# Optimization experiments

Hardware: AMD Instinct MI355X
Metric: run time of the kernel (lower is better)

Reference implementation:

```python
import jax, jax.numpy as jnp
import numpy as np

IN_F = 1024
OUT_F = 1024
GRID_SIZE = 8
GRID_LO, GRID_HI = -2.0, 2.0


def _grid_and_inv_denom():
    grid = jnp.linspace(GRID_LO, GRID_HI, GRID_SIZE)  # [G]
    inv_denom = 1.0 / (float((GRID_HI - GRID_LO) / (GRID_SIZE - 1)) + 1e-06)
    return grid, inv_denom


def setup_inputs() -> dict:
    key = jax.random.key(0)
    kx, kw, ks = jax.random.split(key, 3)
    x = jax.random.normal(kx, (4, 2048, IN_F), dtype=jnp.float32)
    # kaiming_uniform_(a=sqrt(5)) on [out,in]: bound = sqrt(6/((1+a^2)*fan_in)) = sqrt(1/fan_in)
    bound = float(np.sqrt(1.0 / IN_F))
    base_w = jax.random.uniform(kw, (OUT_F, IN_F), minval=-bound, maxval=bound, dtype=jnp.float32)
    base_b = jnp.zeros((OUT_F,), dtype=jnp.float32)
    spline_w = 0.02 * jax.random.normal(ks, (OUT_F, IN_F, GRID_SIZE), dtype=jnp.float32)
    return {"x": x, "base_w": base_w, "base_b": base_b, "spline_w": spline_w}


def reference(x, base_w, base_b, spline_w):
    grid, inv_denom = _grid_and_inv_denom()
    lead = x.shape[:-1]
    x_flat = x.reshape(-1, IN_F)  # [B, in]
    # base path: Linear(SiLU(x))
    base_out = jax.nn.silu(x_flat) @ base_w.T + base_b  # [B, out]
    # RBF basis expansion: [B, in, G]
    basis = jnp.exp(-(((x_flat[..., None] - grid) * inv_denom) ** 2))
    spline_out = jnp.einsum('big,oig->bo', basis, spline_w)  # [B, out]
    out = base_out + spline_out
    return out.reshape(*lead, OUT_F)
```

## Files before the change

### kernel.cpp

```cpp
#include <hip/hip_runtime.h>
#include <stdint.h>

namespace {

constexpr int IN_F = 1024;
constexpr int OUT_F = 1024;
constexpr int GSZ = 8;
constexpr int KTOT = IN_F + IN_F * GSZ;
constexpr int BK = 64;
constexpr int NT = KTOT / BK;
constexpr int NBASE = IN_F / BK;

constexpr int BM = 128, BN = 256;
constexpr int NBLK = OUT_F / BN;
constexpr size_t IMG_BYTES = (size_t)BN * BK * 2;
constexpr size_t WS_NEEDED = (size_t)NBLK * NT * IMG_BYTES;

constexpr double H_D     = 4.0 / 7.0;
constexpr double INVD_D  = 1.0 / (H_D + 1e-6);
constexpr double L2E_D   = 1.4426950408889634;
constexpr double SQL2E_D = 1.2011224087864498;
constexpr double CS_D    = INVD_D * SQL2E_D;
constexpr double DLT_D   = H_D * CS_D;

using short8 = __attribute__((ext_vector_type(8))) short;
using f32x4  = __attribute__((ext_vector_type(4))) float;

__device__ __forceinline__ unsigned cvt_pk(float lo, float hi) {
  unsigned r;
  asm("v_cvt_pk_bf16_f32 %0, %1, %2" : "=v"(r) : "v"(lo), "v"(hi));
  return r;
}
__device__ __forceinline__ float silu_f(float v) {
  float e = __builtin_amdgcn_exp2f(-v * (float)L2E_D);
  return v * __builtin_amdgcn_rcpf(1.0f + e);
}
__device__ __forceinline__ int swz(int row, int kk) {
  return (row * 128 + kk * 2) ^ ((row & 7) << 4);
}

__global__ void wprep(const float* __restrict__ bw, const float* __restrict__ sw,
                      char* __restrict__ wimg)
{
  const int total = NBLK * NT * BN * 8;
  for (int idx = blockIdx.x * blockDim.x + threadIdx.x; idx < total;
       idx += gridDim.x * blockDim.x) {
    const int kk8  = idx & 7;
    const int row  = (idx >> 3) & (BN - 1);
    const int rest = idx >> 11;
    const int step = rest % NT;
    const int nb   = rest / NT;
    const int o    = nb * BN + row;
    const int k    = step * BK + kk8 * 8;
    const float* src = (k < IN_F)
      ? (bw + (size_t)o * IN_F + k)
      : (sw + (size_t)o * (size_t)(IN_F * GSZ) + (k - IN_F));
    const float4 a = ((const float4*)src)[0];
    const float4 b = ((const float4*)src)[1];
    int4 v;
    v.x = (int)cvt_pk(a.x, a.y);
    v.y = (int)cvt_pk(a.z, a.w);
    v.z = (int)cvt_pk(b.x, b.y);
    v.w = (int)cvt_pk(b.z, b.w);
    *(int4*)(wimg + (size_t)rest * IMG_BYTES + swz(row, kk8 * 8)) = v;
  }
}

__global__ __launch_bounds__(512, 2)
void kan_fast(const float* __restrict__ x, const float* __restrict__ bb,
              const char* __restrict__ wimg, float* __restrict__ out)
{
  __shared__ char tA[2][BM * BK * 2];
  __shared__ char tB[2][BN * BK * 2];

  const int t    = threadIdx.x;
  const int lane = t & 63;
  const int wid  = t >> 6;
  const int wr   = (wid >> 2) * 64;
  const int wc   = (wid & 3) * 64;
  const int bm0  = blockIdx.y * BM;
  const char* img = wimg + (size_t)blockIdx.x * NT * IMG_BYTES;
  const int bn0  = blockIdx.x * BN;

  const float CSf  = (float)CS_D;
  const float C0f  = (float)(-2.0 * CS_D);
  const float TDLT = (float)(2.0 * DLT_D);
  float Kc[7];
#pragma unroll
  for (int g = 0; g < 7; ++g) {
    const double cg  = (-2.0 + g * H_D) * CS_D;
    const double cg1 = (-2.0 + (g + 1) * H_D) * CS_D;
    Kc[g] = __builtin_amdgcn_exp2f((float)(-DLT_D * (cg + cg1)));
  }

  f32x4 acc[4][4];
#pragma unroll
  for (int m = 0; m < 4; ++m)
#pragma unroll
    for (int n = 0; n < 4; ++n) acc[m][n] = (f32x4)0.0f;

  float4 xE[4], xO[4];

  auto issue_B2 = [&](int step, char* dstB, int half) {
    const char* g = img + (size_t)step * IMG_BYTES + half * 16384 + t * 16;
    char* l = dstB + half * 16384 + t * 16;
#pragma unroll
    for (int j = 0; j < 2; ++j)
      __builtin_amdgcn_global_load_lds(
        (const __attribute__((address_space(1))) void*)(g + j * 8192),
        (__attribute__((address_space(3))) void*)(l + j * 8192), 16, 0, 0);
  };

  auto load_x = [&](int step, float4 (&xr)[4]) {
    const int k0  = step * BK;
    const int row = t >> 2;
    if (k0 < IN_F) {
      const float* p = x + (size_t)(bm0 + row) * IN_F + k0 + (t & 3) * 16;
#pragma unroll
      for (int j = 0; j < 4; ++j) xr[j] = ((const float4*)p)[j];
    } else {
      const int i0 = (k0 - IN_F) >> 3;
      const float2 v = *(const float2*)(x + (size_t)(bm0 + row) * IN_F + i0 + (t & 3) * 2);
      xr[0].x = v.x; xr[0].y = v.y;
    }
  };

  auto conv_A = [&](int step, const float4 (&xr)[4], char* dstA) {
    const int row = t >> 2;
    if (step < NBASE) {
      unsigned q[8];
#pragma unroll
      for (int j = 0; j < 4; ++j) {
        q[2 * j]     = cvt_pk(silu_f(xr[j].x), silu_f(xr[j].y));
        q[2 * j + 1] = cvt_pk(silu_f(xr[j].z), silu_f(xr[j].w));
      }
      const int kc0 = (t & 3) * 16;
      *(int4*)(dstA + swz(row, kc0))     = make_int4(q[0], q[1], q[2], q[3]);
      *(int4*)(dstA + swz(row, kc0 + 8)) = make_int4(q[4], q[5], q[6], q[7]);
    } else {
#pragma unroll
      for (int c = 0; c < 2; ++c) {
        const float xv = c ? xr[0].y : xr[0].x;
        const float tb = xv * CSf;
        const float d0 = tb - C0f;
        float e = __builtin_amdgcn_exp2f(-(d0 * d0));
        const float r = __builtin_amdgcn_exp2f(tb * TDLT);
        unsigned q[4];
#pragma unroll
        for (int g = 0; g < 4; ++g) {
          const float a = e;
          const float b = a * r * Kc[2 * g];
          q[g] = cvt_pk(a, b);
          if (g < 3) e = b * r * Kc[2 * g + 1];
        }
        const int iloc = (t & 3) * 2 + c;
        *(int4*)(dstA + swz(row, iloc * 8)) = make_int4(q[0], q[1], q[2], q[3]);
      }
    }
  };

  auto read_frags = [&](const char* A, const char* B, int kh,
                        short8 (&af)[4], short8 (&bf)[4]) {
    const int r  = lane & 15;
    const int kq = (lane >> 4) * 8;
#pragma unroll
    for (int m = 0; m < 4; ++m)
      af[m] = *(const short8*)(A + swz(wr + m * 16 + r, kh * 32 + kq));
#pragma unroll
    for (int n = 0; n < 4; ++n)
      bf[n] = *(const short8*)(B + swz(wc + n * 16 + r, kh * 32 + kq));
  };

  auto mfma16 = [&](short8 (&af)[4], short8 (&bf)[4]) {
#pragma unroll
    for (int m = 0; m < 4; ++m)
#pragma unroll
      for (int n = 0; n < 4; ++n)
        acc[m][n] = __builtin_amdgcn_mfma_f32_16x16x32_bf16(af[m], bf[n], acc[m][n], 0, 0, 0);
  };

  auto step_body = [&](int s, char* curA, char* curB, char* nxtA, char* nxtB,
                       const float4 (&xconv)[4], float4 (&xload)[4]) {
    if (s + 1 < NT) issue_B2(s + 1, nxtB, 0);
    if (s + 2 < NT) load_x(s + 2, xload);
    {
      short8 af[4], bf[4];
      read_frags(curA, curB, 0, af, bf);
      __builtin_amdgcn_s_barrier();
      asm volatile("s_waitcnt lgkmcnt(0)" ::: "memory");
      __builtin_amdgcn_sched_barrier(0);
      __builtin_amdgcn_s_setprio(1);
      mfma16(af, bf);
      __builtin_amdgcn_s_setprio(0);
      __builtin_amdgcn_s_barrier();
    }
    if (s + 1 < NT) {
      issue_B2(s + 1, nxtB, 1);
      conv_A(s + 1, xconv, nxtA);
    }
    {
      short8 af[4], bf[4];
      read_frags(curA, curB, 1, af, bf);
      __builtin_amdgcn_s_barrier();
      asm volatile("s_waitcnt lgkmcnt(0)" ::: "memory");
      __builtin_amdgcn_sched_barrier(0);
      __builtin_amdgcn_s_setprio(1);
      mfma16(af, bf);
      __builtin_amdgcn_s_setprio(0);
    }
    __syncthreads();
  };

  load_x(0, xE);
  load_x(1, xO);
  issue_B2(0, tB[0], 0);
  issue_B2(0, tB[0], 1);
  conv_A(0, xE, tA[0]);
  __syncthreads();

  for (int s = 0; s < NT; s += 2) {
    step_body(s,     tA[0], tB[0], tA[1], tB[1], xO, xE);
    step_body(s + 1, tA[1], tB[1], tA[0], tB[0], xE, xO);
  }

  const int col = lane & 15;
  const int rr  = (lane >> 4) * 4;
#pragma unroll
  for (int m = 0; m < 4; ++m) {
    const int gr = bm0 + wr + m * 16 + rr;
#pragma unroll
    for (int n = 0; n < 4; ++n) {
      const int gc = bn0 + wc + n * 16 + col;
      const float bias = bb[gc];
#pragma unroll
      for (int j = 0; j < 4; ++j)
        out[(size_t)(gr + j) * OUT_F + gc] = acc[m][n][j] + bias;
    }
  }
}

constexpr int SLDK = 64 + 8;

__device__ __forceinline__ unsigned f2bf(float f) {
  unsigned u = __float_as_uint(f);
  return (u + 0x7fffu + ((u >> 16) & 1u)) >> 16;
}
__device__ __forceinline__ unsigned pk2(float lo, float hi) {
  return f2bf(lo) | (f2bf(hi) << 16);
}

__global__ __launch_bounds__(256)
void kan_slow(const float* __restrict__ x, const float* __restrict__ bw,
              const float* __restrict__ bb, const float* __restrict__ sw,
              float* __restrict__ out)
{
  __shared__ unsigned short tA[128][SLDK];
  __shared__ unsigned short tB[128][SLDK];

  const int t    = threadIdx.x;
  const int lane = t & 63;
  const int wid  = t >> 6;
  const int wr   = (wid >> 1) * 64;
  const int wc   = (wid & 1) * 64;
  const int bm0  = blockIdx.x * 128;
  const int bn0  = blockIdx.y * 128;

  const float CS = (float)CS_D;
  float gsc[GSZ];
#pragma unroll
  for (int g = 0; g < GSZ; ++g)
    gsc[g] = (float)((-2.0 + g * H_D) * CS_D);

  f32x4 acc[4][4];
#pragma unroll
  for (int m = 0; m < 4; ++m)
#pragma unroll
    for (int n = 0; n < 4; ++n) acc[m][n] = (f32x4)0.0f;

  float4 rA[8], rB[8];
  const int rw = t >> 4;
  const int cw = (t & 15) * 4;

  auto load_tile = [&](int step) {
    const int k0 = step * BK;
    const bool base = (k0 < IN_F);
#pragma unroll
    for (int j = 0; j < 8; ++j) {
      const int row = j * 16 + rw;
      const float* p = base
        ? (bw + (size_t)(bn0 + row) * IN_F + k0 + cw)
        : (sw + (size_t)(bn0 + row) * (size_t)(IN_F * GSZ) + (k0 - IN_F) + cw);
      rB[j] = *(const float4*)p;
    }
    if (base) {
#pragma unroll
      for (int j = 0; j < 8; ++j) {
        const int row = j * 16 + rw;
        rA[j] = *(const float4*)(x + (size_t)(bm0 + row) * IN_F + k0 + cw);
      }
    } else {
      const int i0  = (k0 - IN_F) >> 3;
      const int row = t >> 1;
      rA[0] = *(const float4*)(x + (size_t)(bm0 + row) * IN_F + i0 + (t & 1) * 4);
    }
  };

  auto store_tile = [&](int step) {
    const int k0 = step * BK;
    const bool base = (k0 < IN_F);
#pragma unroll
    for (int j = 0; j < 8; ++j) {
      const int row = j * 16 + rw;
      uint2 v;
      v.x = pk2(rB[j].x, rB[j].y);
      v.y = pk2(rB[j].z, rB[j].w);
      *(uint2*)&tB[row][cw] = v;
    }
    if (base) {
#pragma unroll
      for (int j = 0; j < 8; ++j) {
        const int row = j * 16 + rw;
        uint2 v;
        v.x = pk2(silu_f(rA[j].x), silu_f(rA[j].y));
        v.y = pk2(silu_f(rA[j].z), silu_f(rA[j].w));
        *(uint2*)&tA[row][cw] = v;
      }
    } else {
      const int row  = t >> 1;
      const int half = t & 1;
      const float* xv = (const float*)&rA[0];
#pragma unroll
      for (int c = 0; c < 4; ++c) {
        const float tb = xv[c] * CS;
        union { unsigned u[4]; int4 v4; } pkv;
#pragma unroll
        for (int g = 0; g < 8; g += 2) {
          const float t0 = tb - gsc[g];
          const float t1 = tb - gsc[g + 1];
          const float e0 = __builtin_amdgcn_exp2f(-(t0 * t0));
          const float e1 = __builtin_amdgcn_exp2f(-(t1 * t1));
          pkv.u[g >> 1] = pk2(e0, e1);
        }
        const int kc = (half * 4 + c) * 8;
        *(int4*)&tA[row][kc] = pkv.v4;
      }
    }
  };

  auto compute_tile = [&]() {
    const int r  = lane & 15;
    const int kq = (lane >> 4) * 8;
#pragma unroll
    for (int kh = 0; kh < 2; ++kh) {
      short8 af[4], bf[4];
#pragma unroll
      for (int m = 0; m < 4; ++m)
        af[m] = *(const short8*)&tA[wr + m * 16 + r][kh * 32 + kq];
#pragma unroll
      for (int n = 0; n < 4; ++n)
        bf[n] = *(const short8*)&tB[wc + n * 16 + r][kh * 32 + kq];
#pragma unroll
      for (int m = 0; m < 4; ++m)
#pragma unroll
        for (int n = 0; n < 4; ++n)
          acc[m][n] = __builtin_amdgcn_mfma_f32_16x16x32_bf16(af[m], bf[n], acc[m][n], 0, 0, 0);
    }
  };

  load_tile(0);
  for (int step = 0; step < NT; ++step) {
    store_tile(step);
    __syncthreads();
    if (step + 1 < NT) load_tile(step + 1);
    compute_tile();
    __syncthreads();
  }

  const int col = lane & 15;
  const int rr  = (lane >> 4) * 4;
#pragma unroll
  for (int m = 0; m < 4; ++m) {
    const int gr = bm0 + wr + m * 16 + rr;
#pragma unroll
    for (int n = 0; n < 4; ++n) {
      const int gc = bn0 + wc + n * 16 + col;
      const float bias = bb[gc];
#pragma unroll
      for (int j = 0; j < 4; ++j)
        out[(size_t)(gr + j) * OUT_F + gc] = acc[m][n][j] + bias;
    }
  }
}

}

extern "C" void kernel_launch(void* const* d_in, const int* in_sizes, int n_in,
                              void* d_out, int out_size, void* d_ws, size_t ws_size,
                              hipStream_t stream) {
  const float *x, *bw, *bb, *sw;
  if (in_sizes[0] == OUT_F) {
    bb = (const float*)d_in[0];
    bw = (const float*)d_in[1];
    sw = (const float*)d_in[2];
    x  = (const float*)d_in[3];
  } else {
    x  = (const float*)d_in[0];
    bw = (const float*)d_in[1];
    bb = (const float*)d_in[2];
    sw = (const float*)d_in[3];
  }
  float* out = (float*)d_out;
  const int rows = (in_sizes[0] == OUT_F) ? in_sizes[3] / IN_F : in_sizes[0] / IN_F;

  if (ws_size >= WS_NEEDED && d_ws != nullptr && (rows % BM) == 0) {
    hipLaunchKernelGGL(wprep, dim3(2048), dim3(256), 0, stream, bw, sw, (char*)d_ws);
    dim3 grid(NBLK, rows / BM);
    hipLaunchKernelGGL(kan_fast, grid, dim3(512), 0, stream,
                       x, bb, (const char*)d_ws, out);
  } else {
    dim3 grid(rows / 128, OUT_F / 128);
    hipLaunchKernelGGL(kan_slow, grid, dim3(256), 0, stream, x, bw, bb, sw, out);
  }
}
```

Measured before the change: 187.7 us.

## Halve M tile to 64 rows with 4-wave blocks and single-buffered A tile

Shrinks the block tile from 128x256 to 64x256, with 256 threads per block where each wave owns a 64-column slice. This doubles the number of blocks in the grid. The A tile drops from two LDS buffers to one, so the basis/SiLU conversion now runs after the MFMAs behind an extra __syncthreads rather than overlapping with them. B images are loaded in one call per step. The intent is a smaller LDS and register footprint and more blocks for occupancy, at the cost of twice the global B traffic per output and a serialized A-conversion phase.

Result: slower. 203.4 us (+8.4%).

```diff
diff --git a/kernel.cpp b/kernel.cpp
--- a/kernel.cpp
+++ b/kernel.cpp
@@ -11,7 +11,7 @@
 constexpr int NT = KTOT / BK;
 constexpr int NBASE = IN_F / BK;
 
-constexpr int BM = 128, BN = 256;
+constexpr int BM = 64, BN = 256;
 constexpr int NBLK = OUT_F / BN;
 constexpr size_t IMG_BYTES = (size_t)BN * BK * 2;
 constexpr size_t WS_NEEDED = (size_t)NBLK * NT * IMG_BYTES;
@@ -66,18 +66,17 @@
   }
 }
 
-__global__ __launch_bounds__(512, 2)
+__global__ __launch_bounds__(256, 2)
 void kan_fast(const float* __restrict__ x, const float* __restrict__ bb,
               const char* __restrict__ wimg, float* __restrict__ out)
 {
-  __shared__ char tA[2][BM * BK * 2];
+  __shared__ char tA[BM * BK * 2];
   __shared__ char tB[2][BN * BK * 2];
 
   const int t    = threadIdx.x;
   const int lane = t & 63;
   const int wid  = t >> 6;
-  const int wr   = (wid >> 2) * 64;
-  const int wc   = (wid & 3) * 64;
+  const int wc   = wid * 64;
   const int bm0  = blockIdx.y * BM;
   const char* img = wimg + (size_t)blockIdx.x * NT * IMG_BYTES;
   const int bn0  = blockIdx.x * BN;
@@ -101,14 +100,14 @@
 
   float4 xE[4], xO[4];
 
-  auto issue_B2 = [&](int step, char* dstB, int half) {
-    const char* g = img + (size_t)step * IMG_BYTES + half * 16384 + t * 16;
-    char* l = dstB + half * 16384 + t * 16;
-#pragma unroll
-    for (int j = 0; j < 2; ++j)
+  auto issue_B = [&](int step, char* dstB) {
+    const char* g = img + (size_t)step * IMG_BYTES + t * 16;
+    char* l = dstB + t * 16;
+#pragma unroll
+    for (int j = 0; j < 8; ++j)
       __builtin_amdgcn_global_load_lds(
-        (const __attribute__((address_space(1))) void*)(g + j * 8192),
-        (__attribute__((address_space(3))) void*)(l + j * 8192), 16, 0, 0);
+        (const __attribute__((address_space(1))) void*)(g + j * 4096),
+        (__attribute__((address_space(3))) void*)(l + j * 4096), 16, 0, 0);
   };
 
   auto load_x = [&](int step, float4 (&xr)[4]) {
@@ -125,7 +124,7 @@
     }
   };
 
-  auto conv_A = [&](int step, const float4 (&xr)[4], char* dstA) {
+  auto conv_A = [&](int step, const float4 (&xr)[4]) {
     const int row = t >> 2;
     if (step < NBASE) {
       unsigned q[8];
@@ -135,37 +134,44 @@
         q[2 * j + 1] = cvt_pk(silu_f(xr[j].z), silu_f(xr[j].w));
       }
       const int kc0 = (t & 3) * 16;
-      *(int4*)(dstA + swz(row, kc0))     = make_int4(q[0], q[1], q[2], q[3]);
-      *(int4*)(dstA + swz(row, kc0 + 8)) = make_int4(q[4], q[5], q[6], q[7]);
+      *(int4*)(tA + swz(row, kc0))     = make_int4(q[0], q[1], q[2], q[3]);
+      *(int4*)(tA + swz(row, kc0 + 8)) = make_int4(q[4], q[5], q[6], q[7]);
     } else {
-#pragma unroll
-      for (int c = 0; c < 2; ++c) {
-        const float xv = c ? xr[0].y : xr[0].x;
-        const float tb = xv * CSf;
-        const float d0 = tb - C0f;
-        float e = __builtin_amdgcn_exp2f(-(d0 * d0));
-        const float r = __builtin_amdgcn_exp2f(tb * TDLT);
-        unsigned q[4];
-#pragma unroll
-        for (int g = 0; g < 4; ++g) {
-          const float a = e;
-          const float b = a * r * Kc[2 * g];
-          q[g] = cvt_pk(a, b);
-          if (g < 3) e = b * r * Kc[2 * g + 1];
+      float2 xv; xv.x = xr[0].x; xv.y = xr[0].y;
+      float2 tb; tb.x = xv.x * CSf;        tb.y = xv.y * CSf;
+      float2 d0; d0.x = tb.x - C0f;        d0.y = tb.y - C0f;
+      float2 e;
+      e.x = __builtin_amdgcn_exp2f(-(d0.x * d0.x));
+      e.y = __builtin_amdgcn_exp2f(-(d0.y * d0.y));
+      float2 r;
+      r.x = __builtin_amdgcn_exp2f(tb.x * TDLT);
+      r.y = __builtin_amdgcn_exp2f(tb.y * TDLT);
+      unsigned q0[4], q1[4];
+#pragma unroll
+      for (int g = 0; g < 4; ++g) {
+        float2 a = e;
+        float2 b;
+        b.x = a.x * r.x * Kc[2 * g];
+        b.y = a.y * r.y * Kc[2 * g];
+        q0[g] = cvt_pk(a.x, b.x);
+        q1[g] = cvt_pk(a.y, b.y);
+        if (g < 3) {
+          e.x = b.x * r.x * Kc[2 * g + 1];
+          e.y = b.y * r.y * Kc[2 * g + 1];
         }
-        const int iloc = (t & 3) * 2 + c;
-        *(int4*)(dstA + swz(row, iloc * 8)) = make_int4(q[0], q[1], q[2], q[3]);
       }
-    }
-  };
-
-  auto read_frags = [&](const char* A, const char* B, int kh,
-                        short8 (&af)[4], short8 (&bf)[4]) {
+      const int iloc = (t & 3) * 2;
+      *(int4*)(tA + swz(row, iloc * 8))       = make_int4(q0[0], q0[1], q0[2], q0[3]);
+      *(int4*)(tA + swz(row, (iloc + 1) * 8)) = make_int4(q1[0], q1[1], q1[2], q1[3]);
+    }
+  };
+
+  auto read_frags = [&](const char* B, int kh, short8 (&af)[4], short8 (&bf)[4]) {
     const int r  = lane & 15;
     const int kq = (lane >> 4) * 8;
 #pragma unroll
     for (int m = 0; m < 4; ++m)
-      af[m] = *(const short8*)(A + swz(wr + m * 16 + r, kh * 32 + kq));
+      af[m] = *(const short8*)(tA + swz(m * 16 + r, kh * 32 + kq));
 #pragma unroll
     for (int n = 0; n < 4; ++n)
       bf[n] = *(const short8*)(B + swz(wc + n * 16 + r, kh * 32 + kq));
@@ -179,13 +185,13 @@
         acc[m][n] = __builtin_amdgcn_mfma_f32_16x16x32_bf16(af[m], bf[n], acc[m][n], 0, 0, 0);
   };
 
-  auto step_body = [&](int s, char* curA, char* curB, char* nxtA, char* nxtB,
+  auto step_body = [&](int s, char* curB, char* nxtB,
                        const float4 (&xconv)[4], float4 (&xload)[4]) {
-    if (s + 1 < NT) issue_B2(s + 1, nxtB, 0);
+    if (s + 1 < NT) issue_B(s + 1, nxtB);
     if (s + 2 < NT) load_x(s + 2, xload);
     {
       short8 af[4], bf[4];
-      read_frags(curA, curB, 0, af, bf);
+      read_frags(curB, 0, af, bf);
       __builtin_amdgcn_s_barrier();
       asm volatile("s_waitcnt lgkmcnt(0)" ::: "memory");
       __builtin_amdgcn_sched_barrier(0);
@@ -194,13 +200,9 @@
       __builtin_amdgcn_s_setprio(0);
       __builtin_amdgcn_s_barrier();
     }
-    if (s + 1 < NT) {
-      issue_B2(s + 1, nxtB, 1);
-      conv_A(s + 1, xconv, nxtA);
-    }
     {
       short8 af[4], bf[4];
-      read_frags(curA, curB, 1, af, bf);
+      read_frags(curB, 1, af, bf);
       __builtin_amdgcn_s_barrier();
       asm volatile("s_waitcnt lgkmcnt(0)" ::: "memory");
       __builtin_amdgcn_sched_barrier(0);
@@ -209,25 +211,26 @@
       __builtin_amdgcn_s_setprio(0);
     }
     __syncthreads();
+    if (s + 1 < NT) conv_A(s + 1, xconv);
+    __syncthreads();
   };
 
   load_x(0, xE);
   load_x(1, xO);
-  issue_B2(0, tB[0], 0);
-  issue_B2(0, tB[0], 1);
-  conv_A(0, xE, tA[0]);
+  issue_B(0, tB[0]);
+  conv_A(0, xE);
   __syncthreads();
 
   for (int s = 0; s < NT; s += 2) {
-    step_body(s,     tA[0], tB[0], tA[1], tB[1], xO, xE);
-    step_body(s + 1, tA[1], tB[1], tA[0], tB[0], xE, xO);
+    step_body(s,     tB[0], tB[1], xO, xE);
+    step_body(s + 1, tB[1], tB[0], xE, xO);
   }
 
   const int col = lane & 15;
   const int rr  = (lane >> 4) * 4;
 #pragma unroll
   for (int m = 0; m < 4; ++m) {
-    const int gr = bm0 + wr + m * 16 + rr;
+    const int gr = bm0 + m * 16 + rr;
 #pragma unroll
     for (int n = 0; n < 4; ++n) {
       const int gc = bn0 + wc + n * 16 + col;
@@ -415,7 +418,7 @@
   if (ws_size >= WS_NEEDED && d_ws != nullptr && (rows % BM) == 0) {
     hipLaunchKernelGGL(wprep, dim3(2048), dim3(256), 0, stream, bw, sw, (char*)d_ws);
     dim3 grid(NBLK, rows / BM);
-    hipLaunchKernelGGL(kan_fast, grid, dim3(512), 0, stream,
+    hipLaunchKernelGGL(kan_fast, grid, dim3(256), 0, stream,
                        x, bb, (const char*)d_ws, out);
   } else {
     dim3 grid(rows / 128, OUT_F / 128);
```

## Load B fragments straight to registers, halve M tile, remap block order

Applied to the files above, without the earlier changes.

Drops the LDS staging of the preprocessed weight image. Each wave now loads its B fragments directly from global memory into registers, double-buffered across steps, so B needs no LDS traffic or extra barriers. The block tile shrinks from 128x256 with 512 threads to 64x256 with 256 threads, and a 1D grid is remapped so that adjacent blocks share the same weight column block for cache reuse. The cost is more global and L2 reads of the weights, since each M-tile now reads B directly and M tiles are smaller, plus higher register pressure.

Measured after the change: 191.2 us. About the same (+1.9%).

```diff
diff --git a/kernel.cpp b/kernel.cpp
--- a/kernel.cpp
+++ b/kernel.cpp
@@ -11,7 +11,7 @@
 constexpr int NT = KTOT / BK;
 constexpr int NBASE = IN_F / BK;
 
-constexpr int BM = 128, BN = 256;
+constexpr int BM = 64, BN = 256;
 constexpr int NBLK = OUT_F / BN;
 constexpr size_t IMG_BYTES = (size_t)BN * BK * 2;
 constexpr size_t WS_NEEDED = (size_t)NBLK * NT * IMG_BYTES;
@@ -66,21 +66,24 @@
   }
 }
 
-__global__ __launch_bounds__(512, 2)
+__global__ __launch_bounds__(256, 2)
 void kan_fast(const float* __restrict__ x, const float* __restrict__ bb,
               const char* __restrict__ wimg, float* __restrict__ out)
 {
   __shared__ char tA[2][BM * BK * 2];
-  __shared__ char tB[2][BN * BK * 2];
 
   const int t    = threadIdx.x;
   const int lane = t & 63;
   const int wid  = t >> 6;
-  const int wr   = (wid >> 2) * 64;
-  const int wc   = (wid & 3) * 64;
-  const int bm0  = blockIdx.y * BM;
-  const char* img = wimg + (size_t)blockIdx.x * NT * IMG_BYTES;
-  const int bn0  = blockIdx.x * BN;
+  const int wc   = wid * 64;
+
+  const int d   = blockIdx.x;
+  const int r8  = d & 7;
+  const int nb  = r8 >> 1;
+  const int my  = ((d >> 3) << 1) | (r8 & 1);
+  const int bm0 = my * BM;
+  const int bn0 = nb * BN;
+  const char* img = wimg + (size_t)nb * NT * IMG_BYTES;
 
   const float CSf  = (float)CS_D;
   const float C0f  = (float)(-2.0 * CS_D);
@@ -99,34 +102,43 @@
 #pragma unroll
     for (int n = 0; n < 4; ++n) acc[m][n] = (f32x4)0.0f;
 
+  const int fr = lane & 15;
+  const int kq = (lane >> 4) * 8;
+
+  int boff[8];
+#pragma unroll
+  for (int n = 0; n < 4; ++n)
+#pragma unroll
+    for (int kh = 0; kh < 2; ++kh)
+      boff[n * 2 + kh] = swz(wc + n * 16 + fr, kh * 32 + kq);
+
+  short8 bE[8], bO[8];
   float4 xE[4], xO[4];
 
-  auto issue_B2 = [&](int step, char* dstB, int half) {
-    const char* g = img + (size_t)step * IMG_BYTES + half * 16384 + t * 16;
-    char* l = dstB + half * 16384 + t * 16;
-#pragma unroll
-    for (int j = 0; j < 2; ++j)
-      __builtin_amdgcn_global_load_lds(
-        (const __attribute__((address_space(1))) void*)(g + j * 8192),
-        (__attribute__((address_space(3))) void*)(l + j * 8192), 16, 0, 0);
-  };
+  auto issue_B = [&](int step, short8 (&br)[8]) {
+    const char* base = img + (size_t)step * IMG_BYTES;
+#pragma unroll
+    for (int j = 0; j < 8; ++j)
+      br[j] = *(const short8*)(base + boff[j]);
+  };
+
+  const int prow = t >> 2;
+  const int pcol = t & 3;
 
   auto load_x = [&](int step, float4 (&xr)[4]) {
-    const int k0  = step * BK;
-    const int row = t >> 2;
+    const int k0 = step * BK;
     if (k0 < IN_F) {
-      const float* p = x + (size_t)(bm0 + row) * IN_F + k0 + (t & 3) * 16;
+      const float* p = x + (size_t)(bm0 + prow) * IN_F + k0 + pcol * 16;
 #pragma unroll
       for (int j = 0; j < 4; ++j) xr[j] = ((const float4*)p)[j];
     } else {
       const int i0 = (k0 - IN_F) >> 3;
-      const float2 v = *(const float2*)(x + (size_t)(bm0 + row) * IN_F + i0 + (t & 3) * 2);
+      const float2 v = *(const float2*)(x + (size_t)(bm0 + prow) * IN_F + i0 + pcol * 2);
       xr[0].x = v.x; xr[0].y = v.y;
     }
   };
 
   auto conv_A = [&](int step, const float4 (&xr)[4], char* dstA) {
-    const int row = t >> 2;
     if (step < NBASE) {
       unsigned q[8];
 #pragma unroll
@@ -134,9 +146,9 @@
         q[2 * j]     = cvt_pk(silu_f(xr[j].x), silu_f(xr[j].y));
         q[2 * j + 1] = cvt_pk(silu_f(xr[j].z), silu_f(xr[j].w));
       }
-      const int kc0 = (t & 3) * 16;
-      *(int4*)(dstA + swz(row, kc0))     = make_int4(q[0], q[1], q[2], q[3]);
-      *(int4*)(dstA + swz(row, kc0 + 8)) = make_int4(q[4], q[5], q[6], q[7]);
+      const int kc0 = pcol * 16;
+      *(int4*)(dstA + swz(prow, kc0))     = make_int4(q[0], q[1], q[2], q[3]);
+      *(int4*)(dstA + swz(prow, kc0 + 8)) = make_int4(q[4], q[5], q[6], q[7]);
     } else {
 #pragma unroll
       for (int c = 0; c < 2; ++c) {
@@ -153,81 +165,53 @@
           q[g] = cvt_pk(a, b);
           if (g < 3) e = b * r * Kc[2 * g + 1];
         }
-        const int iloc = (t & 3) * 2 + c;
-        *(int4*)(dstA + swz(row, iloc * 8)) = make_int4(q[0], q[1], q[2], q[3]);
+        *(int4*)(dstA + swz(prow, (pcol * 2 + c) * 8)) = make_int4(q[0], q[1], q[2], q[3]);
       }
     }
   };
 
-  auto read_frags = [&](const char* A, const char* B, int kh,
-                        short8 (&af)[4], short8 (&bf)[4]) {
-    const int r  = lane & 15;
-    const int kq = (lane >> 4) * 8;
+  auto step_body = [&](int s, char* curA, char* nxtA,
+                       short8 (&bCur)[8], short8 (&bNxt)[8],
+                       const float4 (&xconv)[4], float4 (&xload)[4]) {
+    if (s + 1 < NT) issue_B(s + 1, bNxt);
+    if (s + 2 < NT) load_x(s + 2, xload);
+    if (s + 1 < NT) conv_A(s + 1, xconv, nxtA);
+    short8 af[4];
 #pragma unroll
     for (int m = 0; m < 4; ++m)
-      af[m] = *(const short8*)(A + swz(wr + m * 16 + r, kh * 32 + kq));
-#pragma unroll
-    for (int n = 0; n < 4; ++n)
-      bf[n] = *(const short8*)(B + swz(wc + n * 16 + r, kh * 32 + kq));
-  };
-
-  auto mfma16 = [&](short8 (&af)[4], short8 (&bf)[4]) {
+      af[m] = *(const short8*)(curA + swz(m * 16 + fr, kq));
 #pragma unroll
     for (int m = 0; m < 4; ++m)
 #pragma unroll
       for (int n = 0; n < 4; ++n)
-        acc[m][n] = __builtin_amdgcn_mfma_f32_16x16x32_bf16(af[m], bf[n], acc[m][n], 0, 0, 0);
-  };
-
-  auto step_body = [&](int s, char* curA, char* curB, char* nxtA, char* nxtB,
-                       const float4 (&xconv)[4], float4 (&xload)[4]) {
-    if (s + 1 < NT) issue_B2(s + 1, nxtB, 0);
-    if (s + 2 < NT) load_x(s + 2, xload);
-    {
-      short8 af[4], bf[4];
-      read_frags(curA, curB, 0, af, bf);
-      __builtin_amdgcn_s_barrier();
-      asm volatile("s_waitcnt lgkmcnt(0)" ::: "memory");
-      __builtin_amdgcn_sched_barrier(0);
-      __builtin_amdgcn_s_setprio(1);
-      mfma16(af, bf);
-      __builtin_amdgcn_s_setprio(0);
-      __builtin_amdgcn_s_barrier();
-    }
-    if (s + 1 < NT) {
-      issue_B2(s + 1, nxtB, 1);
-      conv_A(s + 1, xconv, nxtA);
-    }
-    {
-      short8 af[4], bf[4];
-      read_frags(curA, curB, 1, af, bf);
-      __builtin_amdgcn_s_barrier();
-      asm volatile("s_waitcnt lgkmcnt(0)" ::: "memory");
-      __builtin_amdgcn_sched_barrier(0);
-      __builtin_amdgcn_s_setprio(1);
-      mfma16(af, bf);
-      __builtin_amdgcn_s_setprio(0);
-    }
+        acc[m][n] = __builtin_amdgcn_mfma_f32_16x16x32_bf16(af[m], bCur[n * 2], acc[m][n], 0, 0, 0);
+#pragma unroll
+    for (int m = 0; m < 4; ++m)
+      af[m] = *(const short8*)(curA + swz(m * 16 + fr, 32 + kq));
+#pragma unroll
+    for (int m = 0; m < 4; ++m)
+#pragma unroll
+      for (int n = 0; n < 4; ++n)
+        acc[m][n] = __builtin_amdgcn_mfma_f32_16x16x32_bf16(af[m], bCur[n * 2 + 1], acc[m][n], 0, 0, 0);
     __syncthreads();
   };
 
   load_x(0, xE);
   load_x(1, xO);
-  issue_B2(0, tB[0], 0);
-  issue_B2(0, tB[0], 1);
+  issue_B(0, bE);
   conv_A(0, xE, tA[0]);
   __syncthreads();
 
   for (int s = 0; s < NT; s += 2) {
-    step_body(s,     tA[0], tB[0], tA[1], tB[1], xO, xE);
-    step_body(s + 1, tA[1], tB[1], tA[0], tB[0], xE, xO);
+    step_body(s,     tA[0], tA[1], bE, bO, xO, xE);
+    step_body(s + 1, tA[1], tA[0], bO, bE, xE, xO);
   }
 
   const int col = lane & 15;
   const int rr  = (lane >> 4) * 4;
 #pragma unroll
   for (int m = 0; m < 4; ++m) {
-    const int gr = bm0 + wr + m * 16 + rr;
+    const int gr = bm0 + m * 16 + rr;
 #pragma unroll
     for (int n = 0; n < 4; ++n) {
       const int gc = bn0 + wc + n * 16 + col;
@@ -412,10 +396,10 @@
   float* out = (float*)d_out;
   const int rows = (in_sizes[0] == OUT_F) ? in_sizes[3] / IN_F : in_sizes[0] / IN_F;
 
-  if (ws_size >= WS_NEEDED && d_ws != nullptr && (rows % BM) == 0) {
+  if (ws_size >= WS_NEEDED && d_ws != nullptr && (rows % (2 * BM)) == 0) {
     hipLaunchKernelGGL(wprep, dim3(2048), dim3(256), 0, stream, bw, sw, (char*)d_ws);
-    dim3 grid(NBLK, rows / BM);
-    hipLaunchKernelGGL(kan_fast, grid, dim3(512), 0, stream,
+    const int nblocks = NBLK * (rows / BM);
+    hipLaunchKernelGGL(kan_fast, dim3(nblocks), dim3(256), 0, stream,
                        x, bb, (const char*)d_ws, out);
   } else {
     dim3 grid(rows / 128, OUT_F / 128);
```
